# Kernel tuning notes

Measured on AMD Instinct MI355X. Metric: run time of the kernel, lower is better.

Reference implementation:

```python
import jax, jax.numpy as jnp
import numpy as np

B, S, H, NH = 8, 512, 1024, 16
HD = H // NH          # 64
MAXP = 512            # max_position_embeddings


def setup_inputs() -> dict:
    key = jax.random.key(0)
    ks = jax.random.split(key, 6)
    sc = 0.02
    return {
        "hidden_states": jax.random.normal(ks[0], (B, S, H), jnp.float32),
        "attention_mask": jnp.zeros((B, 1, 1, S), jnp.float32),
        "Wq": jax.random.normal(ks[1], (H, H), jnp.float32) * sc,
        "bq": jnp.zeros((H,), jnp.float32),
        "Wk": jax.random.normal(ks[2], (H, H), jnp.float32) * sc,
        "bk": jnp.zeros((H,), jnp.float32),
        "Wv": jax.random.normal(ks[3], (H, H), jnp.float32) * sc,
        "bv": jnp.zeros((H,), jnp.float32),
        "dist_emb": jax.random.normal(ks[4], (2 * MAXP - 1, HD), jnp.float32) * sc,
    }


def reference(hidden_states, attention_mask, Wq, bq, Wk, bk, Wv, bv, dist_emb):
    b, s, h = hidden_states.shape
    nh, hd = NH, h // NH

    def heads(x):  # [b,s,h] -> [b,nh,s,hd]
        return x.reshape(b, s, nh, hd).transpose(0, 2, 1, 3)

    q = heads(hidden_states @ Wq.T + bq)
    k = heads(hidden_states @ Wk.T + bk)
    v = heads(hidden_states @ Wv.T + bv)

    # raw QK^T scores [b,nh,s,s]
    scores = jnp.einsum("bhld,bhrd->bhlr", q, k)

    # relative_key positional bias
    dist = jnp.arange(s)[:, None] - jnp.arange(s)[None, :] + (MAXP - 1)
    pos = dist_emb[dist]  # [s,s,hd]
    scores = scores + jnp.einsum("bhld,lrd->bhlr", q, pos)

    scores = scores / jnp.sqrt(jnp.asarray(hd, scores.dtype))
    scores = scores + attention_mask  # additive mask, broadcasts [b,1,1,s]

    probs = jax.nn.softmax(scores, axis=-1)  # dropout p=0 (eval)
    ctx = jnp.einsum("bhlr,bhrd->bhld", probs, v)
    ctx = ctx.transpose(0, 2, 1, 3).reshape(b, s, h)
    return ctx
```

## Files before the change

kernel.cpp:

```cpp
#include <hip/hip_runtime.h>

#define BB 8
#define SS 512
#define HH 1024
#define NHH 16
#define HDD 64

typedef short short8 __attribute__((ext_vector_type(8)));
typedef float f32x4 __attribute__((ext_vector_type(4)));

union U4S8 { unsigned u[4]; short8 s; uint4 v; };

__device__ __forceinline__ void split2(float f0, float f1,
                                       unsigned& hi, unsigned& lo)
{
    unsigned u0 = __builtin_bit_cast(unsigned, f0);
    unsigned u1 = __builtin_bit_cast(unsigned, f1);
    hi = __builtin_amdgcn_perm(u1, u0, 0x07060302u);
    float r0 = f0 - __builtin_bit_cast(float, u0 & 0xffff0000u);
    float r1 = f1 - __builtin_bit_cast(float, u1 & 0xffff0000u);
    unsigned v0 = __builtin_bit_cast(unsigned, r0);
    unsigned v1 = __builtin_bit_cast(unsigned, r1);
    lo = __builtin_amdgcn_perm(v1, v0, 0x07060302u);
}

__device__ __forceinline__ unsigned short bf16_rne(float f) {
    unsigned u = __builtin_bit_cast(unsigned, f);
    u += 0x7fffu + ((u >> 16) & 1u);
    return (unsigned short)(u >> 16);
}
__device__ __forceinline__ unsigned short bf16_tr(float f) {
    return (unsigned short)(__builtin_bit_cast(unsigned, f) >> 16);
}
__device__ __forceinline__ float bf16f(unsigned short s) {
    unsigned u = ((unsigned)s) << 16;
    return __builtin_bit_cast(float, u);
}
__device__ __forceinline__ int swel(int row, int col) {
    return row * 64 + ((((col >> 3) ^ (row & 7)) << 3) | (col & 7));
}

__global__ __launch_bounds__(256)
void qkv_proj_kernel(const float* __restrict__ HS,
                     const float* __restrict__ Wq, const float* __restrict__ bq,
                     const float* __restrict__ Wk, const float* __restrict__ bk,
                     const float* __restrict__ Wv, const float* __restrict__ bv,
                     float* __restrict__ Qo, float* __restrict__ Ko, float* __restrict__ Vo)
{
    const int bx = blockIdx.x;
    const int by = blockIdx.y;
    const int z   = bx >> 3;
    const int nf0 = (bx & 7) * 128;
    const int m0  = by * 128;

    const float* W    = (z == 0) ? Wq : (z == 1) ? Wk : Wv;
    const float* bias = (z == 0) ? bq : (z == 1) ? bk : bv;
    float*       Out  = (z == 0) ? Qo : (z == 1) ? Ko : Vo;

    __shared__ short Ah[128][32];
    __shared__ short Al[128][32];
    __shared__ short Bh[128][32];
    __shared__ short Bl[128][32];

    const int tid  = threadIdx.x;
    const int lane = tid & 63;
    const int wave = tid >> 6;
    const int wm   = (wave & 1) * 64;
    const int wn   = (wave >> 1) * 64;

    const int srow = tid >> 1;
    const int skh  = (tid & 1) * 16;

    const int fr    = lane & 15;
    const int kslot = lane >> 4;

    f32x4 acc[4][4];
#pragma unroll
    for (int i = 0; i < 4; i++)
#pragma unroll
        for (int j = 0; j < 4; j++) acc[i][j] = (f32x4)0.0f;

    for (int k0 = 0; k0 < HH; k0 += 32) {
        __syncthreads();
        {
            float ra[16], rb[16];
            const float* pa = HS + (size_t)(m0 + srow) * HH + k0 + skh;
            const float* pb = W + (size_t)(nf0 + srow) * HH + k0 + skh;
#pragma unroll
            for (int u = 0; u < 4; u++) {
                *(float4*)&ra[4 * u] = *(const float4*)(pa + 4 * u);
                *(float4*)&rb[4 * u] = *(const float4*)(pb + 4 * u);
            }
            unsigned ha[8], la[8], hb[8], lb[8];
#pragma unroll
            for (int p = 0; p < 8; p++) {
                split2(ra[2 * p], ra[2 * p + 1], ha[p], la[p]);
                split2(rb[2 * p], rb[2 * p + 1], hb[p], lb[p]);
            }
            *(uint4*)&Ah[srow][skh]     = *(uint4*)&ha[0];
            *(uint4*)&Ah[srow][skh + 8] = *(uint4*)&ha[4];
            *(uint4*)&Al[srow][skh]     = *(uint4*)&la[0];
            *(uint4*)&Al[srow][skh + 8] = *(uint4*)&la[4];
            *(uint4*)&Bh[srow][skh]     = *(uint4*)&hb[0];
            *(uint4*)&Bh[srow][skh + 8] = *(uint4*)&hb[4];
            *(uint4*)&Bl[srow][skh]     = *(uint4*)&lb[0];
            *(uint4*)&Bl[srow][skh + 8] = *(uint4*)&lb[4];
        }
        __syncthreads();

        short8 a_h[4], a_l[4], b_h[4], b_l[4];
#pragma unroll
        for (int i = 0; i < 4; i++) {
            a_h[i] = *(const short8*)&Ah[wm + i * 16 + fr][kslot * 8];
            a_l[i] = *(const short8*)&Al[wm + i * 16 + fr][kslot * 8];
            b_h[i] = *(const short8*)&Bh[wn + i * 16 + fr][kslot * 8];
            b_l[i] = *(const short8*)&Bl[wn + i * 16 + fr][kslot * 8];
        }
#pragma unroll
        for (int i = 0; i < 4; i++)
#pragma unroll
            for (int j = 0; j < 4; j++) {
                acc[i][j] = __builtin_amdgcn_mfma_f32_16x16x32_bf16(a_h[i], b_h[j], acc[i][j], 0, 0, 0);
                acc[i][j] = __builtin_amdgcn_mfma_f32_16x16x32_bf16(a_h[i], b_l[j], acc[i][j], 0, 0, 0);
                acc[i][j] = __builtin_amdgcn_mfma_f32_16x16x32_bf16(a_l[i], b_h[j], acc[i][j], 0, 0, 0);
            }
    }

    const int cn  = lane & 15;
    const int rm4 = (lane >> 4) * 4;
#pragma unroll
    for (int j = 0; j < 4; j++) {
        const int nn = nf0 + wn + j * 16 + cn;
        const int h  = nn >> 6;
        const int hd = nn & 63;
        const float bval = bias[nn];
#pragma unroll
        for (int i = 0; i < 4; i++) {
            const int mmb = m0 + wm + i * 16 + rm4;
            const int bi  = mmb >> 9;
            const int s0  = mmb & 511;
            float* base = Out + (((size_t)(bi * NHH + h) * SS + s0) * HDD + hd);
#pragma unroll
            for (int r = 0; r < 4; r++)
                base[(size_t)r * HDD] = acc[i][j][r] + bval;
        }
    }
}

__global__ __launch_bounds__(512)
void attn_mfma_kernel(const float* __restrict__ Q, const float* __restrict__ K,
                      const float* __restrict__ V, const float* __restrict__ mask,
                      const float* __restrict__ demb, float* __restrict__ out)
{
    const int qt = blockIdx.x, h = blockIdx.y, b = blockIdx.z;
    const int l0 = qt * 64;
    const int tid  = threadIdx.x;
    const int lane = tid & 63;
    const int wave = tid >> 6;
    const int wl = wave >> 2;
    const int wr = wave & 3;
    const int fr = lane & 15;
    const int q4 = lane >> 4;

    __shared__ short Th[64][584];
    __shared__ short KhS[64 * 64], KlS[64 * 64];
    __shared__ short VthS[64 * 64], VtlS[64 * 64];
    __shared__ short PhS[64 * 64], PlS[64 * 64];
    __shared__ float rowsumw[4][64];
    __shared__ float Ms[64];

    const size_t bh = (size_t)(b * NHH + h) * SS * HDD;
    const float* Qb = Q + bh;
    const float* Kb = K + bh;
    const float* Vb = V + bh;

    const f32x4 fz = {0.f, 0.f, 0.f, 0.f};

    short8 qh[4], ql[4];
#pragma unroll
    for (int i = 0; i < 2; i++)
#pragma unroll
        for (int ks = 0; ks < 2; ks++) {
            const float* src = Qb + (size_t)(l0 + wl * 32 + i * 16 + fr) * HDD + ks * 32 + q4 * 8;
            float4 v0 = *(const float4*)src;
            float4 v1 = *(const float4*)(src + 4);
            U4S8 hh, ll;
            split2(v0.x * 0.125f, v0.y * 0.125f, hh.u[0], ll.u[0]);
            split2(v0.z * 0.125f, v0.w * 0.125f, hh.u[1], ll.u[1]);
            split2(v1.x * 0.125f, v1.y * 0.125f, hh.u[2], ll.u[2]);
            split2(v1.z * 0.125f, v1.w * 0.125f, hh.u[3], ll.u[3]);
            qh[i * 2 + ks] = hh.s;
            ql[i * 2 + ks] = ll.s;
        }

    const int srow = tid >> 3;
    const int sd   = (tid & 7) * 8;
    const int sel  = srow * 64 + (((sd >> 3) ^ (srow & 7)) << 3);
    const int brow = wr * 16 + fr;

    for (int jt = 0; jt < 9; jt++) {
        __syncthreads();
        {
            int jrow = l0 + jt * 64 + srow;
            if (jrow > 1022) jrow = 1022;
            const float* src = demb + (size_t)jrow * HDD + sd;
            float4 v0 = *(const float4*)src;
            float4 v1 = *(const float4*)(src + 4);
            U4S8 hh, ll;
            split2(v0.x, v0.y, hh.u[0], ll.u[0]);
            split2(v0.z, v0.w, hh.u[1], ll.u[1]);
            split2(v1.x, v1.y, hh.u[2], ll.u[2]);
            split2(v1.z, v1.w, hh.u[3], ll.u[3]);
            *(uint4*)&KhS[sel] = hh.v;
            *(uint4*)&KlS[sel] = ll.v;
        }
        __syncthreads();

        f32x4 tacc[2]; tacc[0] = fz; tacc[1] = fz;
#pragma unroll
        for (int ks = 0; ks < 2; ks++) {
            const int bel = brow * 64 + ((((ks * 4) + q4) ^ (brow & 7)) << 3);
            short8 dh = *(const short8*)&KhS[bel];
            short8 dl = *(const short8*)&KlS[bel];
#pragma unroll
            for (int i = 0; i < 2; i++) {
                tacc[i] = __builtin_amdgcn_mfma_f32_16x16x32_bf16(qh[i * 2 + ks], dh, tacc[i], 0, 0, 0);
                tacc[i] = __builtin_amdgcn_mfma_f32_16x16x32_bf16(qh[i * 2 + ks], dl, tacc[i], 0, 0, 0);
                tacc[i] = __builtin_amdgcn_mfma_f32_16x16x32_bf16(ql[i * 2 + ks], dh, tacc[i], 0, 0, 0);
            }
        }
#pragma unroll
        for (int i = 0; i < 2; i++)
#pragma unroll
            for (int r = 0; r < 4; r++)
                Th[wl * 32 + i * 16 + q4 * 4 + r][jt * 64 + brow] = (short)bf16_rne(tacc[i][r]);
    }

    f32x4 ctx[2]; ctx[0] = fz; ctx[1] = fz;
    float rs[2][4] = {{0.f, 0.f, 0.f, 0.f}, {0.f, 0.f, 0.f, 0.f}};

    const int vrow = lane;
    const int vd   = wave * 8;

    for (int rt = 0; rt < 8; rt++) {
        const int r0 = rt * 64;
        __syncthreads();

        {
            const float* src = Kb + (size_t)(r0 + srow) * HDD + sd;
            float4 v0 = *(const float4*)src;
            float4 v1 = *(const float4*)(src + 4);
            U4S8 hh, ll;
            split2(v0.x, v0.y, hh.u[0], ll.u[0]);
            split2(v0.z, v0.w, hh.u[1], ll.u[1]);
            split2(v1.x, v1.y, hh.u[2], ll.u[2]);
            split2(v1.z, v1.w, hh.u[3], ll.u[3]);
            *(uint4*)&KhS[sel] = hh.v;
            *(uint4*)&KlS[sel] = ll.v;
        }
        {
            const float* src = Vb + (size_t)(r0 + vrow) * HDD + vd;
            float4 v0 = *(const float4*)src;
            float4 v1 = *(const float4*)(src + 4);
            float vv[8] = {v0.x, v0.y, v0.z, v0.w, v1.x, v1.y, v1.z, v1.w};
#pragma unroll
            for (int u = 0; u < 8; u++) {
                const int d = vd + u;
                unsigned short hb = bf16_tr(vv[u]);
                float lo = vv[u] - bf16f(hb);
                const int el = swel(d, vrow);
                VthS[el] = (short)hb;
                VtlS[el] = (short)bf16_tr(lo);
            }
        }
        if (tid < 64) Ms[tid] = mask[(size_t)b * SS + r0 + tid];
        __syncthreads();

        f32x4 sacc[2]; sacc[0] = fz; sacc[1] = fz;
#pragma unroll
        for (int ks = 0; ks < 2; ks++) {
            const int bel = brow * 64 + ((((ks * 4) + q4) ^ (brow & 7)) << 3);
            short8 kh = *(const short8*)&KhS[bel];
            short8 kl = *(const short8*)&KlS[bel];
#pragma unroll
            for (int i = 0; i < 2; i++) {
                sacc[i] = __builtin_amdgcn_mfma_f32_16x16x32_bf16(qh[i * 2 + ks], kh, sacc[i], 0, 0, 0);
                sacc[i] = __builtin_amdgcn_mfma_f32_16x16x32_bf16(qh[i * 2 + ks], kl, sacc[i], 0, 0, 0);
                sacc[i] = __builtin_amdgcn_mfma_f32_16x16x32_bf16(ql[i * 2 + ks], kh, sacc[i], 0, 0, 0);
            }
        }

#pragma unroll
        for (int i = 0; i < 2; i++)
#pragma unroll
            for (int r = 0; r < 4; r++) {
                const int li = wl * 32 + i * 16 + q4 * 4 + r;
                const int jj = li + 511 - (r0 + brow);
                float logit = sacc[i][r] + bf16f((unsigned short)Th[li][jj]) + Ms[brow];
                float p = __expf(logit);
                rs[i][r] += p;
                unsigned short phb = bf16_tr(p);
                float plo = p - bf16f(phb);
                const int el = swel(li, brow);
                PhS[el] = (short)phb;
                PlS[el] = (short)bf16_tr(plo);
            }
        __syncthreads();

#pragma unroll
        for (int ks = 0; ks < 2; ks++) {
            const int belv = brow * 64 + ((((ks * 4) + q4) ^ (brow & 7)) << 3);
            short8 vh = *(const short8*)&VthS[belv];
            short8 vl = *(const short8*)&VtlS[belv];
#pragma unroll
            for (int i = 0; i < 2; i++) {
                const int arow = wl * 32 + i * 16 + fr;
                const int ael = arow * 64 + ((((ks * 4) + q4) ^ (arow & 7)) << 3);
                short8 ph = *(const short8*)&PhS[ael];
                short8 pl = *(const short8*)&PlS[ael];
                ctx[i] = __builtin_amdgcn_mfma_f32_16x16x32_bf16(ph, vh, ctx[i], 0, 0, 0);
                ctx[i] = __builtin_amdgcn_mfma_f32_16x16x32_bf16(ph, vl, ctx[i], 0, 0, 0);
                ctx[i] = __builtin_amdgcn_mfma_f32_16x16x32_bf16(pl, vh, ctx[i], 0, 0, 0);
            }
        }
    }

#pragma unroll
    for (int i = 0; i < 2; i++)
#pragma unroll
        for (int r = 0; r < 4; r++) {
            float v = rs[i][r];
            v += __shfl_xor(v, 1);
            v += __shfl_xor(v, 2);
            v += __shfl_xor(v, 4);
            v += __shfl_xor(v, 8);
            if (fr == 0) rowsumw[wr][wl * 32 + i * 16 + q4 * 4 + r] = v;
        }
    __syncthreads();

#pragma unroll
    for (int i = 0; i < 2; i++)
#pragma unroll
        for (int r = 0; r < 4; r++) {
            const int li = wl * 32 + i * 16 + q4 * 4 + r;
            const float s = rowsumw[0][li] + rowsumw[1][li] + rowsumw[2][li] + rowsumw[3][li];
            out[((size_t)(b * SS + l0 + li)) * HH + h * HDD + wr * 16 + fr] = ctx[i][r] / s;
        }
}

extern "C" void kernel_launch(void* const* d_in, const int* in_sizes, int n_in,
                              void* d_out, int out_size, void* d_ws, size_t ws_size,
                              hipStream_t stream)
{
    const float* HS   = (const float*)d_in[0];
    const float* mask = (const float*)d_in[1];
    const float* Wq   = (const float*)d_in[2];
    const float* bq   = (const float*)d_in[3];
    const float* Wk   = (const float*)d_in[4];
    const float* bk   = (const float*)d_in[5];
    const float* Wv   = (const float*)d_in[6];
    const float* bv   = (const float*)d_in[7];
    const float* demb = (const float*)d_in[8];
    float* out = (float*)d_out;

    const size_t per = (size_t)BB * NHH * SS * HDD;
    float* Qw = (float*)d_ws;
    float* Kw = Qw + per;
    float* Vw = Kw + per;

    dim3 gp(24, 32);
    qkv_proj_kernel<<<gp, 256, 0, stream>>>(HS, Wq, bq, Wk, bk, Wv, bv, Qw, Kw, Vw);

    dim3 ga(SS / 64, NHH, BB);
    attn_mfma_kernel<<<ga, 512, 0, stream>>>(Qw, Kw, Vw, mask, demb, out);
}
```

Measured before the change: 276.9 us.

## Emit pre-split bf16 Q/K/V from projection and stream positional-bias chunks

The projection kernel now writes Q, K and V as hi/lo bf16 pairs, with the attention scale folded into Q, so the attention kernel no longer re-splits fp32 data on load. The positional-bias table is computed in chunks interleaved with the key-tile loop, kept in a three-slot ring buffer, instead of a full 64x584 upfront pass. The bias product now uses only the high bf16 part of the distance embedding (one MFMA instead of three). This cuts LDS footprint and front-loaded work, and the launch bounds ask for more resident blocks. The trade-off is some lost precision in the bias term and extra indexing logic.

```diff
diff --git a/kernel.cpp b/kernel.cpp
--- a/kernel.cpp
+++ b/kernel.cpp
@@ -8,6 +8,7 @@
 
 typedef short short8 __attribute__((ext_vector_type(8)));
 typedef float f32x4 __attribute__((ext_vector_type(4)));
+typedef unsigned short ushort;
 
 union U4S8 { unsigned u[4]; short8 s; uint4 v; };
 
@@ -24,15 +25,19 @@
     lo = __builtin_amdgcn_perm(v1, v0, 0x07060302u);
 }
 
-__device__ __forceinline__ unsigned short bf16_rne(float f) {
+__device__ __forceinline__ unsigned pack_hi2(float f0, float f1) {
+    return __builtin_amdgcn_perm(__builtin_bit_cast(unsigned, f1),
+                                 __builtin_bit_cast(unsigned, f0), 0x07060302u);
+}
+__device__ __forceinline__ ushort bf16_rne(float f) {
     unsigned u = __builtin_bit_cast(unsigned, f);
     u += 0x7fffu + ((u >> 16) & 1u);
-    return (unsigned short)(u >> 16);
-}
-__device__ __forceinline__ unsigned short bf16_tr(float f) {
-    return (unsigned short)(__builtin_bit_cast(unsigned, f) >> 16);
-}
-__device__ __forceinline__ float bf16f(unsigned short s) {
+    return (ushort)(u >> 16);
+}
+__device__ __forceinline__ ushort bf16_tr(float f) {
+    return (ushort)(__builtin_bit_cast(unsigned, f) >> 16);
+}
+__device__ __forceinline__ float bf16f(ushort s) {
     unsigned u = ((unsigned)s) << 16;
     return __builtin_bit_cast(float, u);
 }
@@ -45,7 +50,9 @@
                      const float* __restrict__ Wq, const float* __restrict__ bq,
                      const float* __restrict__ Wk, const float* __restrict__ bk,
                      const float* __restrict__ Wv, const float* __restrict__ bv,
-                     float* __restrict__ Qo, float* __restrict__ Ko, float* __restrict__ Vo)
+                     ushort* __restrict__ Qh, ushort* __restrict__ Ql,
+                     ushort* __restrict__ Kh, ushort* __restrict__ Kl,
+                     ushort* __restrict__ Vh, ushort* __restrict__ Vl)
 {
     const int bx = blockIdx.x;
     const int by = blockIdx.y;
@@ -55,7 +62,9 @@
 
     const float* W    = (z == 0) ? Wq : (z == 1) ? Wk : Wv;
     const float* bias = (z == 0) ? bq : (z == 1) ? bk : bv;
-    float*       Out  = (z == 0) ? Qo : (z == 1) ? Ko : Vo;
+    ushort* OutH = (z == 0) ? Qh : (z == 1) ? Kh : Vh;
+    ushort* OutL = (z == 0) ? Ql : (z == 1) ? Kl : Vl;
+    const float sc = (z == 0) ? 0.125f : 1.0f;
 
     __shared__ short Ah[128][32];
     __shared__ short Al[128][32];
@@ -139,18 +148,25 @@
             const int mmb = m0 + wm + i * 16 + rm4;
             const int bi  = mmb >> 9;
             const int s0  = mmb & 511;
-            float* base = Out + (((size_t)(bi * NHH + h) * SS + s0) * HDD + hd);
-#pragma unroll
-            for (int r = 0; r < 4; r++)
-                base[(size_t)r * HDD] = acc[i][j][r] + bval;
+            const size_t base = (((size_t)(bi * NHH + h) * SS + s0) * HDD + hd);
+#pragma unroll
+            for (int r = 0; r < 4; r++) {
+                const float val = (acc[i][j][r] + bval) * sc;
+                const ushort hb = bf16_tr(val);
+                const ushort lb2 = bf16_tr(val - bf16f(hb));
+                OutH[base + (size_t)r * HDD] = hb;
+                OutL[base + (size_t)r * HDD] = lb2;
+            }
         }
     }
 }
 
-__global__ __launch_bounds__(512)
-void attn_mfma_kernel(const float* __restrict__ Q, const float* __restrict__ K,
-                      const float* __restrict__ V, const float* __restrict__ mask,
-                      const float* __restrict__ demb, float* __restrict__ out)
+__global__ __launch_bounds__(512, 4)
+void attn_mfma2_kernel(const ushort* __restrict__ Qh, const ushort* __restrict__ Ql,
+                       const ushort* __restrict__ Kh, const ushort* __restrict__ Kl,
+                       const ushort* __restrict__ Vh, const ushort* __restrict__ Vl,
+                       const float* __restrict__ mask, const float* __restrict__ demb,
+                       float* __restrict__ out)
 {
     const int qt = blockIdx.x, h = blockIdx.y, b = blockIdx.z;
     const int l0 = qt * 64;
@@ -161,19 +177,16 @@
     const int wr = wave & 3;
     const int fr = lane & 15;
     const int q4 = lane >> 4;
-
-    __shared__ short Th[64][584];
-    __shared__ short KhS[64 * 64], KlS[64 * 64];
-    __shared__ short VthS[64 * 64], VtlS[64 * 64];
-    __shared__ short PhS[64 * 64], PlS[64 * 64];
+    const int brow = wr * 16 + fr;
+
+    __shared__ short Thf[3 * 64 * 68];
+    __shared__ short KhS[4096], KlS[4096];
+    __shared__ short VthS[4096], VtlS[4096];
+    __shared__ short PhS[4096], PlS[4096];
+    __shared__ float Ms[64];
     __shared__ float rowsumw[4][64];
-    __shared__ float Ms[64];
 
     const size_t bh = (size_t)(b * NHH + h) * SS * HDD;
-    const float* Qb = Q + bh;
-    const float* Kb = K + bh;
-    const float* Vb = V + bh;
-
     const f32x4 fz = {0.f, 0.f, 0.f, 0.f};
 
     short8 qh[4], ql[4];
@@ -181,126 +194,97 @@
     for (int i = 0; i < 2; i++)
 #pragma unroll
         for (int ks = 0; ks < 2; ks++) {
-            const float* src = Qb + (size_t)(l0 + wl * 32 + i * 16 + fr) * HDD + ks * 32 + q4 * 8;
-            float4 v0 = *(const float4*)src;
-            float4 v1 = *(const float4*)(src + 4);
-            U4S8 hh, ll;
-            split2(v0.x * 0.125f, v0.y * 0.125f, hh.u[0], ll.u[0]);
-            split2(v0.z * 0.125f, v0.w * 0.125f, hh.u[1], ll.u[1]);
-            split2(v1.x * 0.125f, v1.y * 0.125f, hh.u[2], ll.u[2]);
-            split2(v1.z * 0.125f, v1.w * 0.125f, hh.u[3], ll.u[3]);
-            qh[i * 2 + ks] = hh.s;
-            ql[i * 2 + ks] = ll.s;
-        }
+            const size_t off = bh + (size_t)(l0 + wl * 32 + i * 16 + fr) * HDD + ks * 32 + q4 * 8;
+            qh[i * 2 + ks] = *(const short8*)(Qh + off);
+            ql[i * 2 + ks] = *(const short8*)(Ql + off);
+        }
+
+    auto chunk = [&](int jt, int slot) {
+        f32x4 tacc[2]; tacc[0] = fz; tacc[1] = fz;
+#pragma unroll
+        for (int ks = 0; ks < 2; ks++) {
+            int jrow = l0 + jt * 64 + brow;
+            if (jrow > 1022) jrow = 1022;
+            const float* ds = demb + (size_t)jrow * HDD + ks * 32 + q4 * 8;
+            float4 v0 = *(const float4*)ds;
+            float4 v1 = *(const float4*)(ds + 4);
+            U4S8 dh;
+            dh.u[0] = pack_hi2(v0.x, v0.y); dh.u[1] = pack_hi2(v0.z, v0.w);
+            dh.u[2] = pack_hi2(v1.x, v1.y); dh.u[3] = pack_hi2(v1.z, v1.w);
+#pragma unroll
+            for (int i = 0; i < 2; i++)
+                tacc[i] = __builtin_amdgcn_mfma_f32_16x16x32_bf16(qh[i * 2 + ks], dh.s, tacc[i], 0, 0, 0);
+        }
+#pragma unroll
+        for (int i = 0; i < 2; i++)
+#pragma unroll
+            for (int r = 0; r < 4; r++)
+                Thf[slot * 4352 + (wl * 32 + i * 16 + q4 * 4 + r) * 68 + brow] = (short)bf16_rne(tacc[i][r]);
+    };
+
+    chunk(8, 2);
+    chunk(7, 1);
+
+    f32x4 ctx[2]; ctx[0] = fz; ctx[1] = fz;
+    float rs[2][4] = {{0.f, 0.f, 0.f, 0.f}, {0.f, 0.f, 0.f, 0.f}};
 
     const int srow = tid >> 3;
     const int sd   = (tid & 7) * 8;
     const int sel  = srow * 64 + (((sd >> 3) ^ (srow & 7)) << 3);
-    const int brow = wr * 16 + fr;
-
-    for (int jt = 0; jt < 9; jt++) {
-        __syncthreads();
+    const int vrow = lane;
+    const int vd   = wave * 8;
+
+    for (int rt = 0; rt < 8; rt++) {
+        const int r0 = rt * 64;
+        __syncthreads();
+
         {
-            int jrow = l0 + jt * 64 + srow;
-            if (jrow > 1022) jrow = 1022;
-            const float* src = demb + (size_t)jrow * HDD + sd;
-            float4 v0 = *(const float4*)src;
-            float4 v1 = *(const float4*)(src + 4);
-            U4S8 hh, ll;
-            split2(v0.x, v0.y, hh.u[0], ll.u[0]);
-            split2(v0.z, v0.w, hh.u[1], ll.u[1]);
-            split2(v1.x, v1.y, hh.u[2], ll.u[2]);
-            split2(v1.z, v1.w, hh.u[3], ll.u[3]);
-            *(uint4*)&KhS[sel] = hh.v;
-            *(uint4*)&KlS[sel] = ll.v;
-        }
-        __syncthreads();
-
-        f32x4 tacc[2]; tacc[0] = fz; tacc[1] = fz;
+            const size_t off = bh + (size_t)(r0 + srow) * HDD + sd;
+            *(uint4*)&KhS[sel] = *(const uint4*)(Kh + off);
+            *(uint4*)&KlS[sel] = *(const uint4*)(Kl + off);
+        }
+        {
+            const size_t off = bh + (size_t)(r0 + vrow) * HDD + vd;
+            short8 vh8 = *(const short8*)(Vh + off);
+            short8 vl8 = *(const short8*)(Vl + off);
+#pragma unroll
+            for (int u = 0; u < 8; u++) {
+                const int el = swel(vd + u, vrow);
+                VthS[el] = vh8[u];
+                VtlS[el] = vl8[u];
+            }
+        }
+        if (tid < 64) Ms[tid] = mask[(size_t)b * SS + r0 + tid];
+        __syncthreads();
+
+        f32x4 sacc[2]; sacc[0] = fz; sacc[1] = fz;
 #pragma unroll
         for (int ks = 0; ks < 2; ks++) {
             const int bel = brow * 64 + ((((ks * 4) + q4) ^ (brow & 7)) << 3);
-            short8 dh = *(const short8*)&KhS[bel];
-            short8 dl = *(const short8*)&KlS[bel];
+            short8 kh8 = *(const short8*)&KhS[bel];
+            short8 kl8 = *(const short8*)&KlS[bel];
 #pragma unroll
             for (int i = 0; i < 2; i++) {
-                tacc[i] = __builtin_amdgcn_mfma_f32_16x16x32_bf16(qh[i * 2 + ks], dh, tacc[i], 0, 0, 0);
-                tacc[i] = __builtin_amdgcn_mfma_f32_16x16x32_bf16(qh[i * 2 + ks], dl, tacc[i], 0, 0, 0);
-                tacc[i] = __builtin_amdgcn_mfma_f32_16x16x32_bf16(ql[i * 2 + ks], dh, tacc[i], 0, 0, 0);
-            }
-        }
+                sacc[i] = __builtin_amdgcn_mfma_f32_16x16x32_bf16(qh[i * 2 + ks], kh8, sacc[i], 0, 0, 0);
+                sacc[i] = __builtin_amdgcn_mfma_f32_16x16x32_bf16(qh[i * 2 + ks], kl8, sacc[i], 0, 0, 0);
+                sacc[i] = __builtin_amdgcn_mfma_f32_16x16x32_bf16(ql[i * 2 + ks], kh8, sacc[i], 0, 0, 0);
+            }
+        }
+
 #pragma unroll
         for (int i = 0; i < 2; i++)
 #pragma unroll
-            for (int r = 0; r < 4; r++)
-                Th[wl * 32 + i * 16 + q4 * 4 + r][jt * 64 + brow] = (short)bf16_rne(tacc[i][r]);
-    }
-
-    f32x4 ctx[2]; ctx[0] = fz; ctx[1] = fz;
-    float rs[2][4] = {{0.f, 0.f, 0.f, 0.f}, {0.f, 0.f, 0.f, 0.f}};
-
-    const int vrow = lane;
-    const int vd   = wave * 8;
-
-    for (int rt = 0; rt < 8; rt++) {
-        const int r0 = rt * 64;
-        __syncthreads();
-
-        {
-            const float* src = Kb + (size_t)(r0 + srow) * HDD + sd;
-            float4 v0 = *(const float4*)src;
-            float4 v1 = *(const float4*)(src + 4);
-            U4S8 hh, ll;
-            split2(v0.x, v0.y, hh.u[0], ll.u[0]);
-            split2(v0.z, v0.w, hh.u[1], ll.u[1]);
-            split2(v1.x, v1.y, hh.u[2], ll.u[2]);
-            split2(v1.z, v1.w, hh.u[3], ll.u[3]);
-            *(uint4*)&KhS[sel] = hh.v;
-            *(uint4*)&KlS[sel] = ll.v;
-        }
-        {
-            const float* src = Vb + (size_t)(r0 + vrow) * HDD + vd;
-            float4 v0 = *(const float4*)src;
-            float4 v1 = *(const float4*)(src + 4);
-            float vv[8] = {v0.x, v0.y, v0.z, v0.w, v1.x, v1.y, v1.z, v1.w};
-#pragma unroll
-            for (int u = 0; u < 8; u++) {
-                const int d = vd + u;
-                unsigned short hb = bf16_tr(vv[u]);
-                float lo = vv[u] - bf16f(hb);
-                const int el = swel(d, vrow);
-                VthS[el] = (short)hb;
-                VtlS[el] = (short)bf16_tr(lo);
-            }
-        }
-        if (tid < 64) Ms[tid] = mask[(size_t)b * SS + r0 + tid];
-        __syncthreads();
-
-        f32x4 sacc[2]; sacc[0] = fz; sacc[1] = fz;
-#pragma unroll
-        for (int ks = 0; ks < 2; ks++) {
-            const int bel = brow * 64 + ((((ks * 4) + q4) ^ (brow & 7)) << 3);
-            short8 kh = *(const short8*)&KhS[bel];
-            short8 kl = *(const short8*)&KlS[bel];
-#pragma unroll
-            for (int i = 0; i < 2; i++) {
-                sacc[i] = __builtin_amdgcn_mfma_f32_16x16x32_bf16(qh[i * 2 + ks], kh, sacc[i], 0, 0, 0);
-                sacc[i] = __builtin_amdgcn_mfma_f32_16x16x32_bf16(qh[i * 2 + ks], kl, sacc[i], 0, 0, 0);
-                sacc[i] = __builtin_amdgcn_mfma_f32_16x16x32_bf16(ql[i * 2 + ks], kh, sacc[i], 0, 0, 0);
-            }
-        }
-
-#pragma unroll
-        for (int i = 0; i < 2; i++)
-#pragma unroll
             for (int r = 0; r < 4; r++) {
-                const int li = wl * 32 + i * 16 + q4 * 4 + r;
-                const int jj = li + 511 - (r0 + brow);
-                float logit = sacc[i][r] + bf16f((unsigned short)Th[li][jj]) + Ms[brow];
-                float p = __expf(logit);
+                const int li  = wl * 32 + i * 16 + q4 * 4 + r;
+                const int jjg = li + 511 - (r0 + brow);
+                const int jt2 = jjg >> 6;
+                const int slot = jt2 - (jt2 >= 3 ? 3 : 0) - (jt2 >= 6 ? 3 : 0);
+                const float tb = bf16f((ushort)Thf[slot * 4352 + li * 68 + (jjg & 63)]);
+                const float logit = sacc[i][r] + tb + Ms[brow];
+                const float p = __expf(logit);
                 rs[i][r] += p;
-                unsigned short phb = bf16_tr(p);
-                float plo = p - bf16f(phb);
+                const ushort phb = bf16_tr(p);
+                const float plo = p - bf16f(phb);
                 const int el = swel(li, brow);
                 PhS[el] = (short)phb;
                 PlS[el] = (short)bf16_tr(plo);
@@ -310,21 +294,27 @@
 #pragma unroll
         for (int ks = 0; ks < 2; ks++) {
             const int belv = brow * 64 + ((((ks * 4) + q4) ^ (brow & 7)) << 3);
-            short8 vh = *(const short8*)&VthS[belv];
-            short8 vl = *(const short8*)&VtlS[belv];
+            short8 vh8 = *(const short8*)&VthS[belv];
+            short8 vl8 = *(const short8*)&VtlS[belv];
 #pragma unroll
             for (int i = 0; i < 2; i++) {
                 const int arow = wl * 32 + i * 16 + fr;
                 const int ael = arow * 64 + ((((ks * 4) + q4) ^ (arow & 7)) << 3);
-                short8 ph = *(const short8*)&PhS[ael];
-                short8 pl = *(const short8*)&PlS[ael];
-                ctx[i] = __builtin_amdgcn_mfma_f32_16x16x32_bf16(ph, vh, ctx[i], 0, 0, 0);
-                ctx[i] = __builtin_amdgcn_mfma_f32_16x16x32_bf16(ph, vl, ctx[i], 0, 0, 0);
-                ctx[i] = __builtin_amdgcn_mfma_f32_16x16x32_bf16(pl, vh, ctx[i], 0, 0, 0);
-            }
+                short8 ph8 = *(const short8*)&PhS[ael];
+                short8 pl8 = *(const short8*)&PlS[ael];
+                ctx[i] = __builtin_amdgcn_mfma_f32_16x16x32_bf16(ph8, vh8, ctx[i], 0, 0, 0);
+                ctx[i] = __builtin_amdgcn_mfma_f32_16x16x32_bf16(ph8, vl8, ctx[i], 0, 0, 0);
+                ctx[i] = __builtin_amdgcn_mfma_f32_16x16x32_bf16(pl8, vh8, ctx[i], 0, 0, 0);
+            }
+        }
+
+        if (rt < 7) {
+            const int jt2 = 6 - rt;
+            chunk(jt2, jt2 % 3);
         }
     }
 
+    __syncthreads();
 #pragma unroll
     for (int i = 0; i < 2; i++)
 #pragma unroll
@@ -364,13 +354,17 @@
     float* out = (float*)d_out;
 
     const size_t per = (size_t)BB * NHH * SS * HDD;
-    float* Qw = (float*)d_ws;
-    float* Kw = Qw + per;
-    float* Vw = Kw + per;
+    ushort* Qh = (ushort*)d_ws;
+    ushort* Ql = Qh + per;
+    ushort* Kh = Ql + per;
+    ushort* Kl = Kh + per;
+    ushort* Vh = Kl + per;
+    ushort* Vl = Vh + per;
 
     dim3 gp(24, 32);
-    qkv_proj_kernel<<<gp, 256, 0, stream>>>(HS, Wq, bq, Wk, bk, Wv, bv, Qw, Kw, Vw);
+    qkv_proj_kernel<<<gp, 256, 0, stream>>>(HS, Wq, bq, Wk, bk, Wv, bv,
+                                            Qh, Ql, Kh, Kl, Vh, Vl);
 
     dim3 ga(SS / 64, NHH, BB);
-    attn_mfma_kernel<<<ga, 512, 0, stream>>>(Qw, Kw, Vw, mask, demb, out);
-}
+    attn_mfma2_kernel<<<ga, 512, 0, stream>>>(Qh, Ql, Kh, Kl, Vh, Vl, mask, demb, out);
+}
```

Result: slower. 290.9 us (+5.1%).
